# Kernel optimization log

Measured on AMD Instinct MI355X. Metric: run time of the kernel, lower is better.

Reference implementation:

```python
import jax, jax.numpy as jnp
import numpy as np

IN_FEATURES = 64
OUT_FEATURES = 64

def setup_inputs() -> dict:
    key = jax.random.key(0)
    kx, kw = jax.random.split(key)
    x = jax.random.normal(kx, (32, 32, 32, IN_FEATURES), dtype=jnp.float32)
    # quadratic weight: [out_features, in_features * in_features]
    W = jax.random.normal(kw, (OUT_FEATURES, IN_FEATURES * IN_FEATURES), dtype=jnp.float32) * 0.02
    return {"x": x, "W": W}

def reference(x, W):
    # Original: outer = x[..., :, None] * x[..., None, :] -> [B,D1,D2,F*F]; then linear(W).
    # Equivalent fused bilinear contraction: out_o = sum_{f,g} x_f x_g W_{o,f,g}
    F_ = x.shape[-1]
    Wr = W.reshape(W.shape[0], F_, F_)  # [O, F, F]
    return jnp.einsum('bacf,bacg,ofg->baco', x, x, Wr)
```

## Files before the change

kernel.cpp:

```cpp
#include <hip/hip_runtime.h>

typedef __attribute__((ext_vector_type(8))) short bf16x8;
typedef __attribute__((ext_vector_type(4))) float f32x4;

constexpr int KPK = 2304;
constexpr int QK  = 576;
constexpr int NCH = 18;

__device__ __forceinline__ unsigned short bf_rne(float f) {
  unsigned u = __float_as_uint(f);
  return (unsigned short)((u + 0x7fffu + ((u >> 16) & 1u)) >> 16);
}

__global__ __launch_bounds__(256) void wprep_kernel(const float* __restrict__ W,
                                                    unsigned short* __restrict__ Wp) {
  int e = blockIdx.x * 256 + threadIdx.x;
  int c = e & 2047;
  int t2 = e >> 11;
  int kq = t2 / 18;
  int j = t2 - kq * 18;
  int nt = c >> 9;
  int q = (c >> 7) & 3;
  int r16 = (c >> 3) & 15;
  int el = c & 7;
  int o = nt * 16 + r16;
  int kl = j * 32 + q * 8 + el;
  int jblk = kl >> 6, i = kl & 63;
  int run1 = 8 - kq;
  int G, F;
  if (jblk < run1) { G = 7 - kq; F = jblk; } else { G = kq; F = jblk - run1; }
  int f = F * 8 + (i >> 3), g = G * 8 + (i & 7);
  float v = W[o * 4096 + f * 64 + g];
  if (F != G) v += W[o * 4096 + g * 64 + f];
  Wp[e] = bf_rne(v);
}

__global__ __launch_bounds__(512, 2) void quad_kernel(const float* __restrict__ x,
                                                      const unsigned short* __restrict__ Wp,
                                                      float* __restrict__ out) {
  __shared__ float xT[8192];
  __shared__ alignas(16) float red[16384];

  const int t = threadIdx.x;
  const int lane = t & 63;
  const int wv = t >> 6;
  const int kq = wv & 3;
  const int ph = wv >> 2;
  const int q = lane >> 4;
  const int r16 = lane & 15;
  const int pxbase = blockIdx.x * 128;

  const char* wsrc = reinterpret_cast<const char*>(Wp) + kq * (NCH * 4096) + lane * 16;

  auto loadB = [&](int j, bf16x8 (&b)[4]) {
#pragma unroll
    for (int nt = 0; nt < 4; ++nt)
      b[nt] = *reinterpret_cast<const bf16x8*>(wsrc + j * 4096 + nt * 1024);
  };

  bf16x8 bufs[3][4];
  loadB(0, bufs[0]);
  loadB(1, bufs[1]);
  loadB(2, bufs[2]);

  {
    const float* xg_ = x + (long)pxbase * 64;
#pragma unroll
    for (int c = 0; c < 4; ++c) {
      int e4 = c * 512 + t;
      int px = e4 >> 4;
      int f0 = (e4 & 15) * 4;
      float4 v = *reinterpret_cast<const float4*>(xg_ + e4 * 4);
      xT[(f0 + 0) * 128 + (px ^ (f0 + 0))] = v.x;
      xT[(f0 + 1) * 128 + (px ^ (f0 + 1))] = v.y;
      xT[(f0 + 2) * 128 + (px ^ (f0 + 2))] = v.z;
      xT[(f0 + 3) * 128 + (px ^ (f0 + 3))] = v.w;
    }
  }
  __syncthreads();

  float xg[4][8];
  auto load_xg = [&](int G) {
#pragma unroll
    for (int m = 0; m < 4; ++m) {
      int px = ph * 64 + m * 16 + r16;
#pragma unroll
      for (int b = 0; b < 8; ++b) {
        int row = G * 8 + b;
        xg[m][b] = xT[row * 128 + (px ^ row)];
      }
    }
  };
  const int run1 = 8 - kq;
  load_xg(7 - kq);

  f32x4 acc[4][4] = {};

#pragma unroll
  for (int j = 0; j < NCH; ++j) {
    if (j == 2 * run1) load_xg(kq);
    {
      const int s = j & 1;
      const int blk = j >> 1;
      const int F = (blk < run1) ? blk : blk - run1;
      const int row = F * 8 + s * 4 + q;
      bf16x8 afr[4];
#pragma unroll
      for (int m = 0; m < 4; ++m) {
        float xf = xT[row * 128 + ((ph * 64 + m * 16 + r16) ^ row)];
        union { unsigned u[4]; bf16x8 v; } pk;
#pragma unroll
        for (int i = 0; i < 4; ++i) {
          unsigned p0 = __float_as_uint(xf * xg[m][2 * i]);
          unsigned p1 = __float_as_uint(xf * xg[m][2 * i + 1]);
          pk.u[i] = __builtin_amdgcn_perm(p1, p0, 0x07060302u);
        }
        afr[m] = pk.v;
      }
#pragma unroll
      for (int nt = 0; nt < 4; ++nt)
#pragma unroll
        for (int m = 0; m < 4; ++m)
          acc[m][nt] = __builtin_amdgcn_mfma_f32_16x16x32_bf16(afr[m], bufs[j % 3][nt],
                                                               acc[m][nt], 0, 0, 0);
    }
    if (j + 3 < NCH) loadB(j + 3, bufs[j % 3]);
  }

#pragma unroll
  for (int r = 0; r < 2; ++r) {
    if (r) __syncthreads();
#pragma unroll
    for (int mm = 0; mm < 2; ++mm)
#pragma unroll
      for (int nt = 0; nt < 4; ++nt)
        *reinterpret_cast<f32x4*>(red + ((ph * 2 + mm) * 4 + kq) * 1024 +
                                  (nt * 16 + r16) * 16 + q * 4) = acc[2 * r + mm][nt];
    __syncthreads();
    {
      const int mm2 = kq >> 1;
      const int h = kq & 1;
      const float* base = red + (ph * 2 + mm2) * 4 * 1024;
#pragma unroll
      for (int nh = 0; nh < 2; ++nh) {
        int nt = h * 2 + nh;
        int off = (nt * 16 + r16) * 16 + q * 4;
        f32x4 ssum = *reinterpret_cast<const f32x4*>(base + off);
#pragma unroll
        for (int w = 1; w < 4; ++w)
          ssum += *reinterpret_cast<const f32x4*>(base + w * 1024 + off);
        long prow = pxbase + ph * 64 + (2 * r + mm2) * 16 + q * 4;
#pragma unroll
        for (int b = 0; b < 4; ++b)
          out[(prow + b) * 64 + nt * 16 + r16] = ssum[b];
      }
    }
  }
}

extern "C" void kernel_launch(void* const* d_in, const int* in_sizes, int n_in,
                              void* d_out, int out_size, void* d_ws, size_t ws_size,
                              hipStream_t stream) {
  const float* x = (const float*)d_in[0];
  const float* W = (const float*)d_in[1];
  float* out = (float*)d_out;
  unsigned short* Wp = (unsigned short*)d_ws;

  hipLaunchKernelGGL(wprep_kernel, dim3(576), dim3(256), 0, stream, W, Wp);
  hipLaunchKernelGGL(quad_kernel, dim3(256), dim3(512), 0, stream, x, Wp, out);
}
```

Measured before the change: 24.09 us.

## Split waves over output halves instead of pixel halves, vectorize output stores

Waves now partition the 64 output features into two halves, each covering all 128 pixels, instead of partitioning pixels. Each wave loads only half of the packed weight fragments per chunk, while it builds A fragments for twice as many pixel tiles. The weight prefetch is deepened to four chunks. The reduction buffer is halved and runs in four rounds, with each thread writing a float4 of consecutive outputs so global stores are coalesced. The cost is duplicated A-fragment construction (xT reads and multiplies) across the two output halves and more registers for xg and acc, which may affect occupancy at 2 blocks per SM.

```diff
diff --git a/kernel.cpp b/kernel.cpp
--- a/kernel.cpp
+++ b/kernel.cpp
@@ -3,8 +3,6 @@
 typedef __attribute__((ext_vector_type(8))) short bf16x8;
 typedef __attribute__((ext_vector_type(4))) float f32x4;
 
-constexpr int KPK = 2304;
-constexpr int QK  = 576;
 constexpr int NCH = 18;
 
 __device__ __forceinline__ unsigned short bf_rne(float f) {
@@ -15,15 +13,15 @@
 __global__ __launch_bounds__(256) void wprep_kernel(const float* __restrict__ W,
                                                     unsigned short* __restrict__ Wp) {
   int e = blockIdx.x * 256 + threadIdx.x;
-  int c = e & 2047;
-  int t2 = e >> 11;
-  int kq = t2 / 18;
-  int j = t2 - kq * 18;
-  int nt = c >> 9;
-  int q = (c >> 7) & 3;
-  int r16 = (c >> 3) & 15;
-  int el = c & 7;
-  int o = nt * 16 + r16;
+  int el = e & 7;
+  int lane = (e >> 3) & 63;
+  int nt2 = (e >> 9) & 1;
+  int nh = (e >> 10) & 1;
+  int jj = e >> 11;
+  int kq = jj / 18;
+  int j = jj - kq * 18;
+  int q = lane >> 4, r16 = lane & 15;
+  int o = nh * 32 + nt2 * 16 + r16;
   int kl = j * 32 + q * 8 + el;
   int jblk = kl >> 6, i = kl & 63;
   int run1 = 8 - kq;
@@ -39,29 +37,25 @@
                                                       const unsigned short* __restrict__ Wp,
                                                       float* __restrict__ out) {
   __shared__ float xT[8192];
-  __shared__ alignas(16) float red[16384];
+  __shared__ alignas(16) float red[8192];
 
   const int t = threadIdx.x;
   const int lane = t & 63;
   const int wv = t >> 6;
   const int kq = wv & 3;
-  const int ph = wv >> 2;
+  const int nh = wv >> 2;
   const int q = lane >> 4;
   const int r16 = lane & 15;
   const int pxbase = blockIdx.x * 128;
 
-  const char* wsrc = reinterpret_cast<const char*>(Wp) + kq * (NCH * 4096) + lane * 16;
+  const char* wsrc = reinterpret_cast<const char*>(Wp) + kq * 73728 + nh * 2048 + lane * 16;
 
-  auto loadB = [&](int j, bf16x8 (&b)[4]) {
-#pragma unroll
-    for (int nt = 0; nt < 4; ++nt)
-      b[nt] = *reinterpret_cast<const bf16x8*>(wsrc + j * 4096 + nt * 1024);
+  bf16x8 bufs[5][2];
+  auto loadB = [&](int j, int slot) {
+    bufs[slot][0] = *reinterpret_cast<const bf16x8*>(wsrc + j * 4096);
+    bufs[slot][1] = *reinterpret_cast<const bf16x8*>(wsrc + j * 4096 + 1024);
   };
-
-  bf16x8 bufs[3][4];
-  loadB(0, bufs[0]);
-  loadB(1, bufs[1]);
-  loadB(2, bufs[2]);
+  loadB(0, 0); loadB(1, 1); loadB(2, 2); loadB(3, 3);
 
   {
     const float* xg_ = x + (long)pxbase * 64;
@@ -79,11 +73,11 @@
   }
   __syncthreads();
 
-  float xg[4][8];
+  float xg[8][8];
   auto load_xg = [&](int G) {
 #pragma unroll
-    for (int m = 0; m < 4; ++m) {
-      int px = ph * 64 + m * 16 + r16;
+    for (int m = 0; m < 8; ++m) {
+      int px = m * 16 + r16;
 #pragma unroll
       for (int b = 0; b < 8; ++b) {
         int row = G * 8 + b;
@@ -94,66 +88,57 @@
   const int run1 = 8 - kq;
   load_xg(7 - kq);
 
-  f32x4 acc[4][4] = {};
+  f32x4 acc[8][2] = {};
 
 #pragma unroll
   for (int j = 0; j < NCH; ++j) {
+    if (j + 4 < NCH) loadB(j + 4, (j + 4) % 5);
     if (j == 2 * run1) load_xg(kq);
-    {
-      const int s = j & 1;
-      const int blk = j >> 1;
-      const int F = (blk < run1) ? blk : blk - run1;
-      const int row = F * 8 + s * 4 + q;
-      bf16x8 afr[4];
+    const int s = j & 1;
+    const int blk = j >> 1;
+    const int F = (blk < run1) ? blk : blk - run1;
+    const int row = F * 8 + s * 4 + q;
+    const int slot = j % 5;
 #pragma unroll
-      for (int m = 0; m < 4; ++m) {
-        float xf = xT[row * 128 + ((ph * 64 + m * 16 + r16) ^ row)];
-        union { unsigned u[4]; bf16x8 v; } pk;
+    for (int m = 0; m < 8; ++m) {
+      float xf = xT[row * 128 + ((m * 16 + r16) ^ row)];
+      union { unsigned u[4]; bf16x8 v; } pk;
 #pragma unroll
-        for (int i = 0; i < 4; ++i) {
-          unsigned p0 = __float_as_uint(xf * xg[m][2 * i]);
-          unsigned p1 = __float_as_uint(xf * xg[m][2 * i + 1]);
-          pk.u[i] = __builtin_amdgcn_perm(p1, p0, 0x07060302u);
-        }
-        afr[m] = pk.v;
+      for (int i = 0; i < 4; ++i) {
+        unsigned p0 = __float_as_uint(xf * xg[m][2 * i]);
+        unsigned p1 = __float_as_uint(xf * xg[m][2 * i + 1]);
+        pk.u[i] = __builtin_amdgcn_perm(p1, p0, 0x07060302u);
       }
-#pragma unroll
-      for (int nt = 0; nt < 4; ++nt)
-#pragma unroll
-        for (int m = 0; m < 4; ++m)
-          acc[m][nt] = __builtin_amdgcn_mfma_f32_16x16x32_bf16(afr[m], bufs[j % 3][nt],
-                                                               acc[m][nt], 0, 0, 0);
+      acc[m][0] = __builtin_amdgcn_mfma_f32_16x16x32_bf16(pk.v, bufs[slot][0], acc[m][0], 0, 0, 0);
+      acc[m][1] = __builtin_amdgcn_mfma_f32_16x16x32_bf16(pk.v, bufs[slot][1], acc[m][1], 0, 0, 0);
     }
-    if (j + 3 < NCH) loadB(j + 3, bufs[j % 3]);
   }
 
 #pragma unroll
-  for (int r = 0; r < 2; ++r) {
+  for (int r = 0; r < 4; ++r) {
     if (r) __syncthreads();
 #pragma unroll
     for (int mm = 0; mm < 2; ++mm)
 #pragma unroll
-      for (int nt = 0; nt < 4; ++nt)
-        *reinterpret_cast<f32x4*>(red + ((ph * 2 + mm) * 4 + kq) * 1024 +
-                                  (nt * 16 + r16) * 16 + q * 4) = acc[2 * r + mm][nt];
+      for (int nt2 = 0; nt2 < 2; ++nt2)
+        *reinterpret_cast<f32x4*>(red + (mm * 4 + kq) * 1024 +
+                                  (nh * 32 + nt2 * 16 + r16) * 16 + q * 4) = acc[2 * r + mm][nt2];
     __syncthreads();
     {
-      const int mm2 = kq >> 1;
-      const int h = kq & 1;
-      const float* base = red + (ph * 2 + mm2) * 4 * 1024;
+      const int mm_r = wv >> 2;
+      const int oq = wv & 3;
+      const int pxl = lane >> 2;
+      const int o4 = oq * 16 + (lane & 3) * 4;
+      f32x4 ssum = {};
 #pragma unroll
-      for (int nh = 0; nh < 2; ++nh) {
-        int nt = h * 2 + nh;
-        int off = (nt * 16 + r16) * 16 + q * 4;
-        f32x4 ssum = *reinterpret_cast<const f32x4*>(base + off);
+      for (int kk = 0; kk < 4; ++kk) {
+        const float* rb = red + (mm_r * 4 + kk) * 1024;
 #pragma unroll
-        for (int w = 1; w < 4; ++w)
-          ssum += *reinterpret_cast<const f32x4*>(base + w * 1024 + off);
-        long prow = pxbase + ph * 64 + (2 * r + mm2) * 16 + q * 4;
-#pragma unroll
-        for (int b = 0; b < 4; ++b)
-          out[(prow + b) * 64 + nt * 16 + r16] = ssum[b];
+        for (int i = 0; i < 4; ++i)
+          ssum[i] += rb[(o4 + i) * 16 + pxl];
       }
+      long px = pxbase + (2 * r + mm_r) * 16 + pxl;
+      *reinterpret_cast<f32x4*>(out + px * 64 + o4) = ssum;
     }
   }
 }
```

New measurement: 32.56 us. 1.35x slower.

## Fuse weight prep into main kernel via cooperative grid sync

Applied to the files above, without the earlier changes.

Merges the weight-packing kernel into the main kernel, launched cooperatively. Each block packs its share of W, stages x into LDS, then waits on a grid-wide sync before the MFMA loop. The aim is to drop the second launch and the gap between kernels. It also adds a bank-conflict swizzle to the LDS index, widens the B register ring from 3 to 4 slots, and issues B prefetches earlier in each iteration. Grid sync costs something, and the larger register use risks occupancy or the cooperative launch limit.

```diff
diff --git a/kernel.cpp b/kernel.cpp
--- a/kernel.cpp
+++ b/kernel.cpp
@@ -1,10 +1,9 @@
 #include <hip/hip_runtime.h>
+#include <hip/hip_cooperative_groups.h>
 
 typedef __attribute__((ext_vector_type(8))) short bf16x8;
 typedef __attribute__((ext_vector_type(4))) float f32x4;
 
-constexpr int KPK = 2304;
-constexpr int QK  = 576;
 constexpr int NCH = 18;
 
 __device__ __forceinline__ unsigned short bf_rne(float f) {
@@ -12,9 +11,8 @@
   return (unsigned short)((u + 0x7fffu + ((u >> 16) & 1u)) >> 16);
 }
 
-__global__ __launch_bounds__(256) void wprep_kernel(const float* __restrict__ W,
-                                                    unsigned short* __restrict__ Wp) {
-  int e = blockIdx.x * 256 + threadIdx.x;
+__device__ __forceinline__ void wprep_one(const float* __restrict__ W,
+                                          unsigned short* __restrict__ Wp, int e) {
   int c = e & 2047;
   int t2 = e >> 11;
   int kq = t2 / 18;
@@ -35,9 +33,14 @@
   Wp[e] = bf_rne(v);
 }
 
-__global__ __launch_bounds__(512, 2) void quad_kernel(const float* __restrict__ x,
-                                                      const unsigned short* __restrict__ Wp,
-                                                      float* __restrict__ out) {
+__device__ __forceinline__ int xidx(int row, int px) {
+  return row * 128 + (px ^ row ^ ((row & 3) << 4));
+}
+
+__global__ __launch_bounds__(512, 2) void fused_kernel(const float* __restrict__ x,
+                                                       const float* __restrict__ W,
+                                                       unsigned short* __restrict__ Wp,
+                                                       float* __restrict__ out) {
   __shared__ float xT[8192];
   __shared__ alignas(16) float red[16384];
 
@@ -50,34 +53,39 @@
   const int r16 = lane & 15;
   const int pxbase = blockIdx.x * 128;
 
-  const char* wsrc = reinterpret_cast<const char*>(Wp) + kq * (NCH * 4096) + lane * 16;
+  const float* xsrc = x + (long)pxbase * 64;
+  float4 xv[4];
+#pragma unroll
+  for (int c = 0; c < 4; ++c)
+    xv[c] = *reinterpret_cast<const float4*>(xsrc + (c * 512 + t) * 4);
 
-  auto loadB = [&](int j, bf16x8 (&b)[4]) {
+  {
+    int base = blockIdx.x * 576;
+    wprep_one(W, Wp, base + t);
+    if (t < 64) wprep_one(W, Wp, base + 512 + t);
+  }
+
+#pragma unroll
+  for (int c = 0; c < 4; ++c) {
+    int e4 = c * 512 + t;
+    int px = e4 >> 4;
+    int f0 = (e4 & 15) * 4;
+    xT[xidx(f0 + 0, px)] = xv[c].x;
+    xT[xidx(f0 + 1, px)] = xv[c].y;
+    xT[xidx(f0 + 2, px)] = xv[c].z;
+    xT[xidx(f0 + 3, px)] = xv[c].w;
+  }
+
+  cooperative_groups::this_grid().sync();
+
+  const char* wsrc = reinterpret_cast<const char*>(Wp) + kq * 73728 + lane * 16;
+  bf16x8 bufs[4][4];
+  auto loadB = [&](int j, int slot) {
 #pragma unroll
     for (int nt = 0; nt < 4; ++nt)
-      b[nt] = *reinterpret_cast<const bf16x8*>(wsrc + j * 4096 + nt * 1024);
+      bufs[slot][nt] = *reinterpret_cast<const bf16x8*>(wsrc + j * 4096 + nt * 1024);
   };
-
-  bf16x8 bufs[3][4];
-  loadB(0, bufs[0]);
-  loadB(1, bufs[1]);
-  loadB(2, bufs[2]);
-
-  {
-    const float* xg_ = x + (long)pxbase * 64;
-#pragma unroll
-    for (int c = 0; c < 4; ++c) {
-      int e4 = c * 512 + t;
-      int px = e4 >> 4;
-      int f0 = (e4 & 15) * 4;
-      float4 v = *reinterpret_cast<const float4*>(xg_ + e4 * 4);
-      xT[(f0 + 0) * 128 + (px ^ (f0 + 0))] = v.x;
-      xT[(f0 + 1) * 128 + (px ^ (f0 + 1))] = v.y;
-      xT[(f0 + 2) * 128 + (px ^ (f0 + 2))] = v.z;
-      xT[(f0 + 3) * 128 + (px ^ (f0 + 3))] = v.w;
-    }
-  }
-  __syncthreads();
+  loadB(0, 0); loadB(1, 1); loadB(2, 2);
 
   float xg[4][8];
   auto load_xg = [&](int G) {
@@ -85,10 +93,8 @@
     for (int m = 0; m < 4; ++m) {
       int px = ph * 64 + m * 16 + r16;
 #pragma unroll
-      for (int b = 0; b < 8; ++b) {
-        int row = G * 8 + b;
-        xg[m][b] = xT[row * 128 + (px ^ row)];
-      }
+      for (int b = 0; b < 8; ++b)
+        xg[m][b] = xT[xidx(G * 8 + b, px)];
     }
   };
   const int run1 = 8 - kq;
@@ -98,33 +104,32 @@
 
 #pragma unroll
   for (int j = 0; j < NCH; ++j) {
+    if (j + 3 < NCH) loadB(j + 3, (j + 3) & 3);
     if (j == 2 * run1) load_xg(kq);
-    {
-      const int s = j & 1;
-      const int blk = j >> 1;
-      const int F = (blk < run1) ? blk : blk - run1;
-      const int row = F * 8 + s * 4 + q;
-      bf16x8 afr[4];
+    const int s = j & 1;
+    const int blk = j >> 1;
+    const int F = (blk < run1) ? blk : blk - run1;
+    const int row = F * 8 + s * 4 + q;
+    const int slot = j & 3;
+    bf16x8 afr[4];
 #pragma unroll
-      for (int m = 0; m < 4; ++m) {
-        float xf = xT[row * 128 + ((ph * 64 + m * 16 + r16) ^ row)];
-        union { unsigned u[4]; bf16x8 v; } pk;
+    for (int m = 0; m < 4; ++m) {
+      float xf = xT[xidx(row, ph * 64 + m * 16 + r16)];
+      union { unsigned u[4]; bf16x8 v; } pk;
 #pragma unroll
-        for (int i = 0; i < 4; ++i) {
-          unsigned p0 = __float_as_uint(xf * xg[m][2 * i]);
-          unsigned p1 = __float_as_uint(xf * xg[m][2 * i + 1]);
-          pk.u[i] = __builtin_amdgcn_perm(p1, p0, 0x07060302u);
-        }
-        afr[m] = pk.v;
+      for (int i = 0; i < 4; ++i) {
+        unsigned p0 = __float_as_uint(xf * xg[m][2 * i]);
+        unsigned p1 = __float_as_uint(xf * xg[m][2 * i + 1]);
+        pk.u[i] = __builtin_amdgcn_perm(p1, p0, 0x07060302u);
       }
+      afr[m] = pk.v;
+    }
 #pragma unroll
-      for (int nt = 0; nt < 4; ++nt)
+    for (int nt = 0; nt < 4; ++nt)
 #pragma unroll
-        for (int m = 0; m < 4; ++m)
-          acc[m][nt] = __builtin_amdgcn_mfma_f32_16x16x32_bf16(afr[m], bufs[j % 3][nt],
-                                                               acc[m][nt], 0, 0, 0);
-    }
-    if (j + 3 < NCH) loadB(j + 3, bufs[j % 3]);
+      for (int m = 0; m < 4; ++m)
+        acc[m][nt] = __builtin_amdgcn_mfma_f32_16x16x32_bf16(afr[m], bufs[slot][nt],
+                                                             acc[m][nt], 0, 0, 0);
   }
 
 #pragma unroll
@@ -133,7 +138,7 @@
 #pragma unroll
     for (int mm = 0; mm < 2; ++mm)
 #pragma unroll
-      for (int nt = 0; nt < 4; ++nt)
+      for (int nt = 0; nt < 2 * 2; ++nt)
         *reinterpret_cast<f32x4*>(red + ((ph * 2 + mm) * 4 + kq) * 1024 +
                                   (nt * 16 + r16) * 16 + q * 4) = acc[2 * r + mm][nt];
     __syncthreads();
@@ -166,6 +171,7 @@
   float* out = (float*)d_out;
   unsigned short* Wp = (unsigned short*)d_ws;
 
-  hipLaunchKernelGGL(wprep_kernel, dim3(576), dim3(256), 0, stream, W, Wp);
-  hipLaunchKernelGGL(quad_kernel, dim3(256), dim3(512), 0, stream, x, Wp, out);
+  void* args[] = {(void*)&x, (void*)&W, (void*)&Wp, (void*)&out};
+  hipLaunchCooperativeKernel((const void*)fused_kernel, dim3(256), dim3(512),
+                             args, 0, stream);
 }
```

Result: slower. 61.39 us (+154.8%).
